# Kernel optimization log

Measured on AMD Instinct MI355X. Metric: run time of the kernel, lower is better.

Reference implementation:

```python
import jax, jax.numpy as jnp
import numpy as np

EPS = 1e-5

def layer_norm(x, gamma, beta):
    m = x.mean(axis=-1, keepdims=True)
    v = ((x - m) ** 2).mean(axis=-1, keepdims=True)  # correction=0
    return (x - m) / jnp.sqrt(v + EPS) * gamma + beta

def setup_inputs() -> dict:
    key = jax.random.key(0)
    B, T, E, H = 2, 2048, 1024, 16
    hd = E // H
    dff = 4 * E
    ks = jax.random.split(key, 10)
    s = 0.02
    return {
        "x": jax.random.normal(ks[0], (B, T, E), jnp.float32),
        "wq": jax.random.normal(ks[1], (H, E, hd), jnp.float32) * s,
        "wk": jax.random.normal(ks[2], (H, E, hd), jnp.float32) * s,
        "wv": jax.random.normal(ks[3], (H, E, hd), jnp.float32) * s,
        "w_proj": jax.random.normal(ks[4], (E, E), jnp.float32) * s,
        "b_proj": jnp.zeros((E,), jnp.float32),
        "gamma1": jnp.ones((E,), jnp.float32),
        "beta1": jnp.zeros((E,), jnp.float32),
        "gamma2": jnp.ones((E,), jnp.float32),
        "beta2": jnp.zeros((E,), jnp.float32),
        "w1": jax.random.normal(ks[5], (E, dff), jnp.float32) * s,
        "b1": jnp.zeros((dff,), jnp.float32),
        "w2": jax.random.normal(ks[6], (dff, E), jnp.float32) * s,
        "b2": jnp.zeros((E,), jnp.float32),
    }

def reference(x, wq, wk, wv, w_proj, b_proj, gamma1, beta1, gamma2, beta2, w1, b1, w2, b2):
    B, T, E = x.shape
    H, _, hd = wq.shape
    # pre-attention norm; NOTE: residual uses the normalized value (as in source)
    h = layer_norm(x, gamma1, beta1)
    # per-head projections, vectorized over heads: [B,H,T,hd]
    q = jnp.einsum('bte,hek->bhtk', h, wq)
    k = jnp.einsum('bte,hek->bhtk', h, wk)
    v = jnp.einsum('bte,hek->bhtk', h, wv)
    att = jnp.einsum('bhtk,bhsk->bhts', q, k) / jnp.sqrt(jnp.float32(hd))
    causal = jnp.tril(jnp.ones((T, T), bool))
    att = jnp.where(causal, att, -jnp.inf)
    p = jax.nn.softmax(att, axis=-1)  # dropout is identity in eval
    o = jnp.einsum('bhts,bhsk->bhtk', p, v)
    o = o.transpose(0, 2, 1, 3).reshape(B, T, E)  # concat heads
    attn_out = o @ w_proj + b_proj
    x2 = h + attn_out
    # pre-FFN norm; residual again uses normalized value
    h2 = layer_norm(x2, gamma2, beta2)
    ffn = jax.nn.relu(h2 @ w1 + b1) @ w2 + b2
    return h2 + ffn
```

## Files before the change

kernel.cpp:

```cpp
#include <hip/hip_runtime.h>
#include <stdint.h>

typedef unsigned short u16;
typedef __attribute__((ext_vector_type(8))) short short8;
typedef __attribute__((ext_vector_type(4))) short short4_t;
typedef __attribute__((ext_vector_type(4))) float f32x4;

__device__ __forceinline__ float b2f(u16 u){ union{unsigned i; float f;}v; v.i=((unsigned)u)<<16; return v.f; }
__device__ __forceinline__ u16 f2b(float f){ unsigned x=__float_as_uint(f); return (u16)((x + 0x7fffu + ((x>>16)&1u))>>16); }

#if __has_builtin(__builtin_amdgcn_exp2f)
#define EXP2F(x) __builtin_amdgcn_exp2f(x)
#else
#define EXP2F(x) exp2f(x)
#endif

#if __has_builtin(__builtin_amdgcn_mfma_f32_16x16x16_bf16)
#define MFMA16(a,b,c) __builtin_amdgcn_mfma_f32_16x16x16_bf16(a,b,c,0,0,0)
#elif __has_builtin(__builtin_amdgcn_mfma_f32_16x16x16bf16_1k)
#define MFMA16(a,b,c) __builtin_amdgcn_mfma_f32_16x16x16bf16_1k(a,b,c,0,0,0)
#else
static __device__ __forceinline__ f32x4 mfma16_asm(short4_t a, short4_t b, f32x4 c){
  __asm__("v_mfma_f32_16x16x16_bf16 %0, %1, %2, %3" : "=v"(c) : "v"(a), "v"(b), "0"(c));
  return c;
}
#define MFMA16(a,b,c) mfma16_asm(a,b,c)
#endif

__device__ __forceinline__ void async16(const void* g, void* l){
  __builtin_amdgcn_global_load_lds((const __attribute__((address_space(1))) void*)g,
                                   (__attribute__((address_space(3))) void*)l, 16, 0, 0);
}

__device__ __forceinline__ short4_t pack4(f32x4 s){
  unsigned u0 = (__float_as_uint(s[0]) + 0x8000u) >> 16;
  unsigned u1 = (__float_as_uint(s[1]) + 0x8000u) & 0xffff0000u;
  unsigned u2 = (__float_as_uint(s[2]) + 0x8000u) >> 16;
  unsigned u3 = (__float_as_uint(s[3]) + 0x8000u) & 0xffff0000u;
  union { unsigned v[2]; short4_t s4; } r;
  r.v[0] = u0 | u1; r.v[1] = u2 | u3;
  return r.s4;
}

template<int IN_F32>
__global__ __launch_bounds__(256) void ln_kernel(const void* __restrict__ xin,
    const float* __restrict__ g, const float* __restrict__ b, u16* __restrict__ y)
{
  const int E = 1024;
  int row = blockIdx.x, t = threadIdx.x;
  float f0,f1,f2,f3;
  if (IN_F32){
    const float* xr = (const float*)xin + (size_t)row*E;
    float4 xv = *(const float4*)(xr + t*4);
    f0=xv.x; f1=xv.y; f2=xv.z; f3=xv.w;
  } else {
    const u16* xr = (const u16*)xin + (size_t)row*E;
    ushort4 xv = *(const ushort4*)(xr + t*4);
    f0=b2f(xv.x); f1=b2f(xv.y); f2=b2f(xv.z); f3=b2f(xv.w);
  }
  float s1 = f0+f1+f2+f3;
  float s2 = f0*f0+f1*f1+f2*f2+f3*f3;
  #pragma unroll
  for (int off=32; off>=1; off>>=1){ s1 += __shfl_xor(s1,off); s2 += __shfl_xor(s2,off); }
  __shared__ float red[8];
  int w = t>>6;
  if ((t&63)==0){ red[w]=s1; red[4+w]=s2; }
  __syncthreads();
  float S1 = red[0]+red[1]+red[2]+red[3];
  float S2 = red[4]+red[5]+red[6]+red[7];
  float mean = S1*(1.0f/E);
  float var  = S2*(1.0f/E) - mean*mean;
  float inv  = rsqrtf(var + 1e-5f);
  float4 gv = *(const float4*)(g + t*4);
  float4 bv = *(const float4*)(b + t*4);
  ushort4 o;
  o.x = f2b((f0-mean)*inv*gv.x+bv.x);
  o.y = f2b((f1-mean)*inv*gv.y+bv.y);
  o.z = f2b((f2-mean)*inv*gv.z+bv.z);
  o.w = f2b((f3-mean)*inv*gv.w+bv.w);
  *(ushort4*)(y + (size_t)row*E + t*4) = o;
}

__global__ __launch_bounds__(256) void transpose_bt(const float* __restrict__ src, u16* __restrict__ dst,
                                                    int ld_src, int ld_dst)
{
  __shared__ u16 tile[64*66];
  int c0 = blockIdx.x*64, r0 = blockIdx.y*64;
  int t = threadIdx.x;
  #pragma unroll
  for (int i=0;i<16;++i){
    int lin = i*256 + t;
    int rr = lin>>6, cc = lin&63;
    tile[cc*66+rr] = f2b(src[(size_t)(r0+rr)*ld_src + c0+cc]);
  }
  __syncthreads();
  #pragma unroll
  for (int i=0;i<16;++i){
    int lin = i*256 + t;
    int cc = lin>>6, rr = lin&63;
    dst[(size_t)(c0+cc)*ld_dst + r0+rr] = tile[cc*66+rr];
  }
}

__global__ __launch_bounds__(256) void qkv_repack(const float* __restrict__ wq, const float* __restrict__ wk,
                                                  const float* __restrict__ wv, u16* __restrict__ dst)
{
  __shared__ u16 tile[64*66];
  int e0 = blockIdx.x*64;
  int sel = blockIdx.y>>4, h = blockIdx.y&15;
  const float* src = (sel==0?wq:(sel==1?wk:wv)) + (size_t)h*1024*64;
  int t = threadIdx.x;
  #pragma unroll
  for (int i=0;i<16;++i){
    int lin=i*256+t; int rr=lin>>6, cc=lin&63;
    tile[cc*66+rr] = f2b(src[(size_t)(e0+rr)*64 + cc]);
  }
  __syncthreads();
  #pragma unroll
  for (int i=0;i<16;++i){
    int lin=i*256+t; int cc=lin>>6, rr=lin&63;
    dst[(size_t)(sel*1024 + h*64 + cc)*1024 + e0+rr] = tile[cc*66+rr];
  }
}

__global__ __launch_bounds__(256) void vtrans(const u16* __restrict__ qkv, u16* __restrict__ VT)
{
  __shared__ u16 tile[64*66];
  int bh = blockIdx.y, bb = bh>>4, h = bh&15;
  int s0 = blockIdx.x*64;
  const u16* src = qkv + ((size_t)(bb*2048) + s0)*3072 + 2048 + h*64;
  int t = threadIdx.x;
  int sr = t>>3, c0 = (t&7)*8;
  #pragma unroll
  for (int half=0; half<2; ++half){
    const u16* p = src + (size_t)(sr+half*32)*3072 + c0;
    ushort4 v0 = *(const ushort4*)p;
    ushort4 v1 = *(const ushort4*)(p+4);
    uint* d = (uint*)(tile + (sr+half*32)*66 + c0);
    d[0] = (uint)v0.x | ((uint)v0.y<<16);
    d[1] = (uint)v0.z | ((uint)v0.w<<16);
    d[2] = (uint)v1.x | ((uint)v1.y<<16);
    d[3] = (uint)v1.z | ((uint)v1.w<<16);
  }
  __syncthreads();
  u16* out = VT + (size_t)bh*64*2048 + s0;
  int dw = t>>3, sc = (t&7)*8;
  #pragma unroll
  for (int half=0; half<2; ++half){
    int d = dw + half*32;
    short8 pk;
    #pragma unroll
    for (int j=0;j<8;++j) pk[j] = (short)tile[(sc+j)*66 + d];
    *(short8*)(out + (size_t)d*2048 + sc) = pk;
  }
}

__global__ __launch_bounds__(256, 4) void gemm64(const u16* __restrict__ A, const u16* __restrict__ Bt,
    u16* __restrict__ C, float* __restrict__ Cf, int M, int N, int K,
    const float* __restrict__ bias, const u16* __restrict__ residual, int do_relu, int gx)
{
  __shared__ __align__(16) u16 As[2][64*64];
  __shared__ __align__(16) u16 Bs[2][64*64];
  int t = threadIdx.x;
  int bid = blockIdx.y * gridDim.x + blockIdx.x;
  int xcd = bid & 7, slot = bid >> 3;
  int gy = 8 / gx;
  int rx = gridDim.x / gx, ry = gridDim.y / gy;
  int col_b = (xcd % gx) * rx + (slot % rx);
  int row_b = (xcd / gx) * ry + (slot / rx);
  int row0 = row_b*64, col0 = col_b*64;
  int l = t&63, w = t>>6;
  int lr = l&15, lq = l>>4;
  (void)M;

  f32x4 acc[4];
  #pragma unroll
  for (int j=0;j<4;++j) acc[j] = f32x4{0.f,0.f,0.f,0.f};

  const u16* gA = A  + (size_t)(row0 + (t>>3))*K + (((t&7)^((t>>3)&7))<<3);
  const u16* gB = Bt + (size_t)(col0 + (t>>3))*K + (((t&7)^((t>>3)&7))<<3);
  const size_t rnd = (size_t)32*K;
  int nk = K>>6;

  #pragma unroll
  for (int r=0;r<2;++r){
    async16(gA + r*rnd, As[0] + r*2048 + t*8);
    async16(gB + r*rnd, Bs[0] + r*2048 + t*8);
  }

  int sw8 = (lr&7);
  for (int kt=0; kt<nk; ++kt){
    int cur = kt&1;
    __syncthreads();
    if (kt+1 < nk){
      int ko = (kt+1)<<6;
      #pragma unroll
      for (int r=0;r<2;++r){
        async16(gA + r*rnd + ko, As[cur^1] + r*2048 + t*8);
        async16(gB + r*rnd + ko, Bs[cur^1] + r*2048 + t*8);
      }
    }
    const u16* as = As[cur];
    const u16* bs = Bs[cur];
    #pragma unroll
    for (int kk=0;kk<2;++kk){
      int so = (((kk*4+lq)^sw8))<<3;
      short8 a = *(const short8*)(as + (w*16+lr)*64 + so);
      short8 b[4];
      #pragma unroll
      for (int j=0;j<4;++j) b[j] = *(const short8*)(bs + (j*16+lr)*64 + so);
      #pragma unroll
      for (int j=0;j<4;++j)
        acc[j] = __builtin_amdgcn_mfma_f32_16x16x32_bf16(a, b[j], acc[j], 0,0,0);
    }
  }

  #pragma unroll
  for (int j=0;j<4;++j){
    int col = col0 + j*16 + lr;
    float bv = bias ? bias[col] : 0.0f;
    #pragma unroll
    for (int r=0;r<4;++r){
      int row = row0 + w*16 + lq*4 + r;
      float v = acc[j][r] + bv;
      if (do_relu) v = fmaxf(v, 0.0f);
      if (residual) v += b2f(residual[(size_t)row*N + col]);
      if (Cf) Cf[(size_t)row*N + col] = v;
      else    C [(size_t)row*N + col] = f2b(v);
    }
  }
}

__global__ __launch_bounds__(512,2) void gemm256(const u16* __restrict__ A, const u16* __restrict__ Bt,
    u16* __restrict__ C, float* __restrict__ Cf, int N, int K,
    const float* __restrict__ bias, const u16* __restrict__ residual, int do_relu, int gx)
{
  __shared__ __align__(16) u16 As[2][256*64];
  __shared__ __align__(16) u16 Bs[2][256*64];
  int t = threadIdx.x;
  int bid = blockIdx.y*gridDim.x + blockIdx.x;
  int xcd = bid & 7, slot = bid >> 3;
  int gy = 8/gx;
  int rx = gridDim.x/gx, ry = gridDim.y/gy;
  int col_b = (xcd%gx)*rx + slot%rx;
  int row_b = (xcd/gx)*ry + slot/rx;
  int row0 = row_b*256, col0 = col_b*256;
  int l = t&63, w = t>>6;
  int wr = w>>2, wc = w&3;
  int lr = l&15, lq = l>>4, sw = lr&7;

  f32x4 acc[8][4];
  #pragma unroll
  for (int m=0;m<8;++m)
    #pragma unroll
    for (int n=0;n<4;++n) acc[m][n] = f32x4{0.f,0.f,0.f,0.f};

  int i = t>>3, c8 = t&7;
  int swc = (c8 ^ (i&7))*8;
  const u16* aS[4]; const u16* bS[4];
  {
    int la[4] = { i, 128+i, 64+i, 192+i };
    #pragma unroll
    for (int s=0;s<4;++s){
      aS[s] = A + (size_t)(row0 + la[s])*K + swc;
      int p = s*64 + i;
      int lb = ((p>>5)&3)*64 + (p>>7)*32 + (p&31);
      bS[s] = Bt + (size_t)(col0 + lb)*K + swc;
    }
  }
  int nk = K>>6;

  u16* A0p = As[0]; u16* A1p = As[1];
  u16* B0p = Bs[0]; u16* B1p = Bs[1];

  short8 af[4][2], bP[2][2], bQ[2][2];

#define VM8  asm volatile("s_waitcnt vmcnt(8)" ::: "memory");
#define VM6  asm volatile("s_waitcnt vmcnt(6)" ::: "memory");
#define VM0  asm volatile("s_waitcnt vmcnt(0)" ::: "memory");
#define BAR  __builtin_amdgcn_s_barrier();

#define RD_A(BUF,qm) \
  _Pragma("unroll") \
  for (int mm=0;mm<4;++mm){ \
    _Pragma("unroll") \
    for (int kk=0;kk<2;++kk) \
      af[mm][kk] = *(const short8*)((const u16*)(BUF) + ((qm)*128 + wr*64 + mm*16 + lr)*64 + (((kk*4+lq)^sw)<<3)); \
  }
#define RD_B(DST,BUF,qn) \
  _Pragma("unroll") \
  for (int nn=0;nn<2;++nn){ \
    _Pragma("unroll") \
    for (int kk=0;kk<2;++kk) \
      DST[nn][kk] = *(const short8*)((const u16*)(BUF) + ((qn)*128 + wc*32 + nn*16 + lr)*64 + (((kk*4+lq)^sw)<<3)); \
  }
#define MMQ(qm,qn,BSS) \
  __builtin_amdgcn_s_setprio(1); \
  _Pragma("unroll") \
  for (int mm=0;mm<4;++mm){ \
    _Pragma("unroll") \
    for (int nn=0;nn<2;++nn){ \
      _Pragma("unroll") \
      for (int kk=0;kk<2;++kk) \
        acc[(qm)*4+mm][(qn)*2+nn] = __builtin_amdgcn_mfma_f32_16x16x32_bf16(af[mm][kk], BSS[nn][kk], acc[(qm)*4+mm][(qn)*2+nn], 0,0,0); \
    } \
  } \
  __builtin_amdgcn_s_setprio(0);

  async16(aS[0], A0p + 0*4096 + t*8);
  async16(aS[1], A0p + 1*4096 + t*8);
  async16(bS[0], B0p + 0*4096 + t*8);
  async16(bS[1], B0p + 1*4096 + t*8);
  async16(bS[2], B0p + 2*4096 + t*8);
  async16(bS[3], B0p + 3*4096 + t*8);
  async16(aS[2], A0p + 2*4096 + t*8);
  async16(aS[3], A0p + 3*4096 + t*8);
  async16(aS[0]+64, A1p + 0*4096 + t*8);
  async16(aS[1]+64, A1p + 1*4096 + t*8);
  async16(bS[0]+64, B1p + 0*4096 + t*8);
  async16(bS[1]+64, B1p + 1*4096 + t*8);
  async16(bS[2]+64, B1p + 2*4096 + t*8);
  async16(bS[3]+64, B1p + 3*4096 + t*8);
  VM8; BAR;
  RD_A(A0p, 0); RD_B(bP, B0p, 0);

  for (int kt=0; kt<nk-1; ++kt){
    int cur = kt&1;
    u16* Ac = As[cur]; u16* Bc = Bs[cur];
    u16* An = As[cur^1]; u16* Bn = Bs[cur^1];
    int ko1 = (kt+1)<<6;
    int kc2 = (kt+2 < nk) ? kt+2 : nk-1;
    int ko2 = kc2<<6;
    async16(aS[2]+ko1, An + 2*4096 + t*8);
    async16(aS[3]+ko1, An + 3*4096 + t*8);
    BAR;
    MMQ(0,0,bP);
    RD_B(bQ, Bc, 1);
    BAR;
    async16(bS[2]+ko2, Bc + 2*4096 + t*8);
    async16(bS[3]+ko2, Bc + 3*4096 + t*8);
    VM8; BAR;
    MMQ(0,1,bQ);
    RD_A(Ac, 1);
    BAR;
    async16(aS[0]+ko2, Ac + 0*4096 + t*8);
    async16(aS[1]+ko2, Ac + 1*4096 + t*8);
    BAR;
    MMQ(1,1,bQ);
    BAR;
    async16(bS[0]+ko2, Bc + 0*4096 + t*8);
    async16(bS[1]+ko2, Bc + 1*4096 + t*8);
    VM8; BAR;
    MMQ(1,0,bP);
    RD_A(An, 0); RD_B(bP, Bn, 0);
    BAR;
  }
  {
    int cur = (nk-1)&1;
    u16* Ac = As[cur]; u16* Bc = Bs[cur];
    BAR;
    MMQ(0,0,bP);
    RD_B(bQ, Bc, 1);
    BAR;
    VM6; BAR;
    MMQ(0,1,bQ);
    RD_A(Ac, 1);
    MMQ(1,1,bQ);
    MMQ(1,0,bP);
  }
  VM0;

#undef VM8
#undef VM6
#undef VM0
#undef BAR
#undef RD_A
#undef RD_B
#undef MMQ

  #pragma unroll
  for (int m=0;m<8;++m){
    #pragma unroll
    for (int n=0;n<4;++n){
      int col = col0 + wc*64 + n*16 + lr;
      float bv = bias ? bias[col] : 0.0f;
      #pragma unroll
      for (int r=0;r<4;++r){
        int row = row0 + wr*128 + m*16 + lq*4 + r;
        float v = acc[m][n][r] + bv;
        if (do_relu) v = fmaxf(v, 0.0f);
        if (residual) v += b2f(residual[(size_t)row*N + col]);
        if (Cf) Cf[(size_t)row*N + col] = v;
        else    C [(size_t)row*N + col] = f2b(v);
      }
    }
  }
}

__global__ __launch_bounds__(256,4) void attn_kernel(const u16* __restrict__ QKV,
    const u16* __restrict__ VT, u16* __restrict__ O)
{
  const int T=2048, LD=3072, E=1024;
  int bid = blockIdx.y * gridDim.x + blockIdx.x;
  int xcd = bid & 7, slot = bid >> 3;
  int idx = slot & 31, grp = slot >> 5;
  int qt = (grp & 1) ? idx : 31 - idx;
  int bh = xcd*4 + grp;
  int bb = bh>>4, h = bh&15;
  const u16* base = QKV + (size_t)bb*T*LD;
  const u16* Qp = base + h*64;
  const u16* Kp = base + 1024 + h*64;
  const u16* Vtp = VT + (size_t)bh*64*2048;
  int t = threadIdx.x, l = t&63, w = t>>6;
  int lr = l&15, lq = l>>4;

  __shared__ __align__(16) u16 Ks[2][64*64];
  __shared__ __align__(16) u16 Vs[2][64*64];

  const float QSC = 0.125f*1.44269504f;
  int q0 = qt*64 + w*16;
  short8 aq[2];
  #pragma unroll
  for (int kk=0;kk<2;++kk){
    short8 raw = *(const short8*)(Qp + (size_t)(q0+lr)*LD + kk*32 + lq*8);
    short8 sc;
    #pragma unroll
    for (int j=0;j<8;++j) sc[j] = (short)f2b(b2f((u16)raw[j])*QSC);
    aq[kk]=sc;
  }

  float mrun = -3e38f, lrun = 0.f;
  f32x4 Oacc[4];
  #pragma unroll
  for (int dt=0;dt<4;++dt) Oacc[dt] = f32x4{0.f,0.f,0.f,0.f};

  int kc = (l&7) ^ (l>>3);
  int ra = 8*w + (l>>3);

  async16(Kp  + (size_t)ra*LD        + kc*8, Ks[0] + t*8);
  async16(Kp  + (size_t)(ra+32)*LD   + kc*8, Ks[0] + 2048 + t*8);
  async16(Vtp + (size_t)ra*2048      + kc*8, Vs[0] + t*8);
  async16(Vtp + (size_t)(ra+32)*2048 + kc*8, Vs[0] + 2048 + t*8);

  for (int it=0; it<=qt; ++it){
    int s0 = it*64, cur = it&1;
    __syncthreads();
    if (it < qt){
      int sn = s0+64;
      u16* kd = Ks[cur^1]; u16* vd = Vs[cur^1];
      async16(Kp  + (size_t)(sn+ra)*LD        + kc*8, kd + t*8);
      async16(Kp  + (size_t)(sn+ra+32)*LD     + kc*8, kd + 2048 + t*8);
      async16(Vtp + (size_t)ra*2048      + sn + kc*8, vd + t*8);
      async16(Vtp + (size_t)(ra+32)*2048 + sn + kc*8, vd + 2048 + t*8);
    }
    const u16* ks = Ks[cur];
    const u16* vs = Vs[cur];

    f32x4 S[4];
    #pragma unroll
    for (int st=0; st<4; ++st){
      short8 kf0 = *(const short8*)(ks + (st*16+lr)*64 + ((lq  )^(lr&7))*8);
      short8 kf1 = *(const short8*)(ks + (st*16+lr)*64 + ((4+lq)^(lr&7))*8);
      f32x4 z = f32x4{0.f,0.f,0.f,0.f};
      z = __builtin_amdgcn_mfma_f32_16x16x32_bf16(kf0, aq[0], z, 0,0,0);
      z = __builtin_amdgcn_mfma_f32_16x16x32_bf16(kf1, aq[1], z, 0,0,0);
      S[st] = z;
    }
    if (it == qt){
      int qg = q0 + lr;
      #pragma unroll
      for (int st=0;st<4;++st)
        #pragma unroll
        for (int r=0;r<4;++r){
          int sg = s0 + st*16 + lq*4 + r;
          if (sg > qg) S[st][r] = -3e38f;
        }
    }
    float m = S[0][0];
    #pragma unroll
    for (int st=0;st<4;++st)
      #pragma unroll
      for (int r=0;r<4;++r) m = fmaxf(m, S[st][r]);
    m = fmaxf(m, __shfl_xor(m,16));
    m = fmaxf(m, __shfl_xor(m,32));
    float mnew = fmaxf(mrun, m);
    float alpha = EXP2F(mrun - mnew);
    mrun = mnew;
    float ssum = 0.f;
    #pragma unroll
    for (int st=0;st<4;++st)
      #pragma unroll
      for (int r=0;r<4;++r){ float p = EXP2F(S[st][r]-mnew); S[st][r]=p; ssum+=p; }
    ssum += __shfl_xor(ssum,16);
    ssum += __shfl_xor(ssum,32);
    lrun = lrun*alpha + ssum;
    short4_t pk[4];
    #pragma unroll
    for (int st=0;st<4;++st) pk[st] = pack4(S[st]);
    float af[4];
    #pragma unroll
    for (int r=0;r<4;++r) af[r] = __shfl(alpha, lq*4+r);
    #pragma unroll
    for (int dt=0;dt<4;++dt)
      #pragma unroll
      for (int r=0;r<4;++r) Oacc[dt][r] *= af[r];
    #pragma unroll
    for (int st=0;st<4;++st){
      #pragma unroll
      for (int dt=0;dt<4;++dt){
        short4_t vf = *(const short4_t*)(vs + (dt*16+lr)*64 + ((2*st+(lq>>1))^(lr&7))*8 + (lq&1)*4);
        Oacc[dt] = MFMA16(pk[st], vf, Oacc[dt]);
      }
    }
  }
  float linv[4];
  #pragma unroll
  for (int r=0;r<4;++r) linv[r] = 1.0f/__shfl(lrun, lq*4+r);
  #pragma unroll
  for (int dt=0;dt<4;++dt)
    #pragma unroll
    for (int r=0;r<4;++r){
      int qg = q0 + lq*4 + r;
      O[(size_t)(bb*T+qg)*E + h*64 + dt*16 + lr] = f2b(Oacc[dt][r]*linv[r]);
    }
}

extern "C" void kernel_launch(void* const* d_in, const int* in_sizes, int n_in,
                              void* d_out, int out_size, void* d_ws, size_t ws_size,
                              hipStream_t stream)
{
  (void)in_sizes; (void)n_in; (void)out_size; (void)ws_size;
  const float* x     = (const float*)d_in[0];
  const float* wq    = (const float*)d_in[1];
  const float* wk    = (const float*)d_in[2];
  const float* wv    = (const float*)d_in[3];
  const float* wproj = (const float*)d_in[4];
  const float* bproj = (const float*)d_in[5];
  const float* g1    = (const float*)d_in[6];
  const float* be1   = (const float*)d_in[7];
  const float* g2    = (const float*)d_in[8];
  const float* be2   = (const float*)d_in[9];
  const float* w1    = (const float*)d_in[10];
  const float* b1    = (const float*)d_in[11];
  const float* w2    = (const float*)d_in[12];
  const float* b2    = (const float*)d_in[13];
  float* out = (float*)d_out;

  char* ws = (char*)d_ws;
  size_t off = 0;
  auto alloc = [&](size_t bytes)->void*{ void* p = ws + off; off += (bytes + 255) & ~(size_t)255; return p; };
  u16* hnorm  = (u16*)alloc((size_t)4096*1024*2);
  u16* qkv    = (u16*)alloc((size_t)4096*3072*2);
  u16* VT     = (u16*)alloc((size_t)32*64*2048*2);
  u16* attnO  = (u16*)alloc((size_t)4096*1024*2);
  u16* x2     = (u16*)alloc((size_t)4096*1024*2);
  u16* h2     = (u16*)alloc((size_t)4096*1024*2);
  u16* ffn1   = (u16*)alloc((size_t)4096*4096*2);
  u16* wqkvT  = (u16*)alloc((size_t)3072*1024*2);
  u16* wprojT = (u16*)alloc((size_t)1024*1024*2);
  u16* w1T    = (u16*)alloc((size_t)4096*1024*2);
  u16* w2T    = (u16*)alloc((size_t)1024*4096*2);

  qkv_repack  <<<dim3(16,48),256,0,stream>>>(wq,wk,wv,wqkvT);
  transpose_bt<<<dim3(16,16),256,0,stream>>>(wproj, wprojT, 1024, 1024);
  transpose_bt<<<dim3(64,16),256,0,stream>>>(w1,    w1T,    4096, 1024);
  transpose_bt<<<dim3(16,64),256,0,stream>>>(w2,    w2T,    1024, 4096);

  ln_kernel<1><<<4096,256,0,stream>>>(x, g1, be1, hnorm);
  gemm256<<<dim3(12,16),512,0,stream>>>(hnorm, wqkvT, qkv, nullptr, 3072, 1024, nullptr, nullptr, 0, 4);
  vtrans<<<dim3(32,32),256,0,stream>>>(qkv, VT);
  attn_kernel<<<dim3(32,32),256,0,stream>>>(qkv, VT, attnO);
  gemm64<<<dim3(16,64),256,0,stream>>>(attnO, wprojT, x2, nullptr, 4096,1024,1024, bproj, hnorm, 0, 4);
  ln_kernel<0><<<4096,256,0,stream>>>(x2, g2, be2, h2);
  gemm256<<<dim3(16,16),512,0,stream>>>(h2, w1T, ffn1, nullptr, 4096, 1024, b1, nullptr, 1, 4);
  gemm64<<<dim3(16,64),256,0,stream>>>(ffn1, w2T, nullptr, out, 4096,1024,4096, b2, h2, 0, 4);
}
```

Baseline: 348.2 us.

## Process two query subtiles per attention block to reuse K/V tiles

```diff
diff --git a/kernel.cpp b/kernel.cpp
--- a/kernel.cpp
+++ b/kernel.cpp
@@ -397,14 +397,14 @@
   }
 }
 
-__global__ __launch_bounds__(256,4) void attn_kernel(const u16* __restrict__ QKV,
+__global__ __launch_bounds__(256,2) void attn_kernel(const u16* __restrict__ QKV,
     const u16* __restrict__ VT, u16* __restrict__ O)
 {
   const int T=2048, LD=3072, E=1024;
   int bid = blockIdx.y * gridDim.x + blockIdx.x;
   int xcd = bid & 7, slot = bid >> 3;
-  int idx = slot & 31, grp = slot >> 5;
-  int qt = (grp & 1) ? idx : 31 - idx;
+  int idx = slot & 15, grp = slot >> 4;
+  int qt = ((grp>>1)&1) ? idx : 15 - idx;
   int bh = xcd*4 + grp;
   int bb = bh>>4, h = bh&15;
   const u16* base = QKV + (size_t)bb*T*LD;
@@ -418,21 +418,26 @@
   __shared__ __align__(16) u16 Vs[2][64*64];
 
   const float QSC = 0.125f*1.44269504f;
-  int q0 = qt*64 + w*16;
-  short8 aq[2];
+  int q0 = qt*128 + w*16;
+  short8 aq0[2], aq1[2];
   #pragma unroll
   for (int kk=0;kk<2;++kk){
-    short8 raw = *(const short8*)(Qp + (size_t)(q0+lr)*LD + kk*32 + lq*8);
-    short8 sc;
-    #pragma unroll
-    for (int j=0;j<8;++j) sc[j] = (short)f2b(b2f((u16)raw[j])*QSC);
-    aq[kk]=sc;
-  }
-
-  float mrun = -3e38f, lrun = 0.f;
-  f32x4 Oacc[4];
-  #pragma unroll
-  for (int dt=0;dt<4;++dt) Oacc[dt] = f32x4{0.f,0.f,0.f,0.f};
+    short8 r0 = *(const short8*)(Qp + (size_t)(q0+lr)*LD    + kk*32 + lq*8);
+    short8 r1 = *(const short8*)(Qp + (size_t)(q0+64+lr)*LD + kk*32 + lq*8);
+    short8 s0v, s1v;
+    #pragma unroll
+    for (int j=0;j<8;++j){
+      s0v[j] = (short)f2b(b2f((u16)r0[j])*QSC);
+      s1v[j] = (short)f2b(b2f((u16)r1[j])*QSC);
+    }
+    aq0[kk]=s0v; aq1[kk]=s1v;
+  }
+
+  float mrun0 = -3e38f, lrun0 = 0.f;
+  float mrun1 = -3e38f, lrun1 = 0.f;
+  f32x4 O0[4], O1[4];
+  #pragma unroll
+  for (int dt=0;dt<4;++dt){ O0[dt] = f32x4{0.f,0.f,0.f,0.f}; O1[dt] = f32x4{0.f,0.f,0.f,0.f}; }
 
   int kc = (l&7) ^ (l>>3);
   int ra = 8*w + (l>>3);
@@ -442,10 +447,11 @@
   async16(Vtp + (size_t)ra*2048      + kc*8, Vs[0] + t*8);
   async16(Vtp + (size_t)(ra+32)*2048 + kc*8, Vs[0] + 2048 + t*8);
 
-  for (int it=0; it<=qt; ++it){
+  int itmax = 2*qt + 1;
+  for (int it=0; it<=itmax; ++it){
     int s0 = it*64, cur = it&1;
     __syncthreads();
-    if (it < qt){
+    if (it < itmax){
       int sn = s0+64;
       u16* kd = Ks[cur^1]; u16* vd = Vs[cur^1];
       async16(Kp  + (size_t)(sn+ra)*LD        + kc*8, kd + t*8);
@@ -456,72 +462,122 @@
     const u16* ks = Ks[cur];
     const u16* vs = Vs[cur];
 
-    f32x4 S[4];
+    f32x4 S0[4], S1[4];
     #pragma unroll
     for (int st=0; st<4; ++st){
       short8 kf0 = *(const short8*)(ks + (st*16+lr)*64 + ((lq  )^(lr&7))*8);
       short8 kf1 = *(const short8*)(ks + (st*16+lr)*64 + ((4+lq)^(lr&7))*8);
-      f32x4 z = f32x4{0.f,0.f,0.f,0.f};
-      z = __builtin_amdgcn_mfma_f32_16x16x32_bf16(kf0, aq[0], z, 0,0,0);
-      z = __builtin_amdgcn_mfma_f32_16x16x32_bf16(kf1, aq[1], z, 0,0,0);
-      S[st] = z;
-    }
-    if (it == qt){
+      f32x4 z0 = f32x4{0.f,0.f,0.f,0.f};
+      f32x4 z1 = f32x4{0.f,0.f,0.f,0.f};
+      z0 = __builtin_amdgcn_mfma_f32_16x16x32_bf16(kf0, aq0[0], z0, 0,0,0);
+      z0 = __builtin_amdgcn_mfma_f32_16x16x32_bf16(kf1, aq0[1], z0, 0,0,0);
+      z1 = __builtin_amdgcn_mfma_f32_16x16x32_bf16(kf0, aq1[0], z1, 0,0,0);
+      z1 = __builtin_amdgcn_mfma_f32_16x16x32_bf16(kf1, aq1[1], z1, 0,0,0);
+      S0[st] = z0; S1[st] = z1;
+    }
+    if (it >= 2*qt){
       int qg = q0 + lr;
       #pragma unroll
       for (int st=0;st<4;++st)
         #pragma unroll
         for (int r=0;r<4;++r){
           int sg = s0 + st*16 + lq*4 + r;
-          if (sg > qg) S[st][r] = -3e38f;
+          if (sg > qg) S0[st][r] = -3e38f;
         }
     }
-    float m = S[0][0];
-    #pragma unroll
-    for (int st=0;st<4;++st)
-      #pragma unroll
-      for (int r=0;r<4;++r) m = fmaxf(m, S[st][r]);
-    m = fmaxf(m, __shfl_xor(m,16));
-    m = fmaxf(m, __shfl_xor(m,32));
-    float mnew = fmaxf(mrun, m);
-    float alpha = EXP2F(mrun - mnew);
-    mrun = mnew;
-    float ssum = 0.f;
-    #pragma unroll
-    for (int st=0;st<4;++st)
-      #pragma unroll
-      for (int r=0;r<4;++r){ float p = EXP2F(S[st][r]-mnew); S[st][r]=p; ssum+=p; }
-    ssum += __shfl_xor(ssum,16);
-    ssum += __shfl_xor(ssum,32);
-    lrun = lrun*alpha + ssum;
-    short4_t pk[4];
-    #pragma unroll
-    for (int st=0;st<4;++st) pk[st] = pack4(S[st]);
-    float af[4];
-    #pragma unroll
-    for (int r=0;r<4;++r) af[r] = __shfl(alpha, lq*4+r);
-    #pragma unroll
-    for (int dt=0;dt<4;++dt)
-      #pragma unroll
-      for (int r=0;r<4;++r) Oacc[dt][r] *= af[r];
+    if (it == itmax){
+      int qg = q0 + 64 + lr;
+      #pragma unroll
+      for (int st=0;st<4;++st)
+        #pragma unroll
+        for (int r=0;r<4;++r){
+          int sg = s0 + st*16 + lq*4 + r;
+          if (sg > qg) S1[st][r] = -3e38f;
+        }
+    }
+    short4_t pk0[4], pk1[4];
+    {
+      float m = S0[0][0];
+      #pragma unroll
+      for (int st=0;st<4;++st)
+        #pragma unroll
+        for (int r=0;r<4;++r) m = fmaxf(m, S0[st][r]);
+      m = fmaxf(m, __shfl_xor(m,16));
+      m = fmaxf(m, __shfl_xor(m,32));
+      float mnew = fmaxf(mrun0, m);
+      float alpha = EXP2F(mrun0 - mnew);
+      mrun0 = mnew;
+      float ssum = 0.f;
+      #pragma unroll
+      for (int st=0;st<4;++st)
+        #pragma unroll
+        for (int r=0;r<4;++r){ float p = EXP2F(S0[st][r]-mnew); S0[st][r]=p; ssum+=p; }
+      ssum += __shfl_xor(ssum,16);
+      ssum += __shfl_xor(ssum,32);
+      lrun0 = lrun0*alpha + ssum;
+      #pragma unroll
+      for (int st=0;st<4;++st) pk0[st] = pack4(S0[st]);
+      float af[4];
+      #pragma unroll
+      for (int r=0;r<4;++r) af[r] = __shfl(alpha, lq*4+r);
+      #pragma unroll
+      for (int dt=0;dt<4;++dt)
+        #pragma unroll
+        for (int r=0;r<4;++r) O0[dt][r] *= af[r];
+    }
+    {
+      float m = S1[0][0];
+      #pragma unroll
+      for (int st=0;st<4;++st)
+        #pragma unroll
+        for (int r=0;r<4;++r) m = fmaxf(m, S1[st][r]);
+      m = fmaxf(m, __shfl_xor(m,16));
+      m = fmaxf(m, __shfl_xor(m,32));
+      float mnew = fmaxf(mrun1, m);
+      float alpha = EXP2F(mrun1 - mnew);
+      mrun1 = mnew;
+      float ssum = 0.f;
+      #pragma unroll
+      for (int st=0;st<4;++st)
+        #pragma unroll
+        for (int r=0;r<4;++r){ float p = EXP2F(S1[st][r]-mnew); S1[st][r]=p; ssum+=p; }
+      ssum += __shfl_xor(ssum,16);
+      ssum += __shfl_xor(ssum,32);
+      lrun1 = lrun1*alpha + ssum;
+      #pragma unroll
+      for (int st=0;st<4;++st) pk1[st] = pack4(S1[st]);
+      float af[4];
+      #pragma unroll
+      for (int r=0;r<4;++r) af[r] = __shfl(alpha, lq*4+r);
+      #pragma unroll
+      for (int dt=0;dt<4;++dt)
+        #pragma unroll
+        for (int r=0;r<4;++r) O1[dt][r] *= af[r];
+    }
     #pragma unroll
     for (int st=0;st<4;++st){
       #pragma unroll
       for (int dt=0;dt<4;++dt){
         short4_t vf = *(const short4_t*)(vs + (dt*16+lr)*64 + ((2*st+(lq>>1))^(lr&7))*8 + (lq&1)*4);
-        Oacc[dt] = MFMA16(pk[st], vf, Oacc[dt]);
+        O0[dt] = MFMA16(pk0[st], vf, O0[dt]);
+        O1[dt] = MFMA16(pk1[st], vf, O1[dt]);
       }
     }
   }
-  float linv[4];
-  #pragma unroll
-  for (int r=0;r<4;++r) linv[r] = 1.0f/__shfl(lrun, lq*4+r);
+  float linv0[4], linv1[4];
+  #pragma unroll
+  for (int r=0;r<4;++r){
+    linv0[r] = 1.0f/__shfl(lrun0, lq*4+r);
+    linv1[r] = 1.0f/__shfl(lrun1, lq*4+r);
+  }
   #pragma unroll
   for (int dt=0;dt<4;++dt)
     #pragma unroll
     for (int r=0;r<4;++r){
-      int qg = q0 + lq*4 + r;
-      O[(size_t)(bb*T+qg)*E + h*64 + dt*16 + lr] = f2b(Oacc[dt][r]*linv[r]);
+      int qa = q0 + lq*4 + r;
+      int qb = q0 + 64 + lq*4 + r;
+      O[(size_t)(bb*T+qa)*E + h*64 + dt*16 + lr] = f2b(O0[dt][r]*linv0[r]);
+      O[(size_t)(bb*T+qb)*E + h*64 + dt*16 + lr] = f2b(O1[dt][r]*linv1[r]);
     }
 }
 
@@ -569,7 +625,7 @@
   ln_kernel<1><<<4096,256,0,stream>>>(x, g1, be1, hnorm);
   gemm256<<<dim3(12,16),512,0,stream>>>(hnorm, wqkvT, qkv, nullptr, 3072, 1024, nullptr, nullptr, 0, 4);
   vtrans<<<dim3(32,32),256,0,stream>>>(qkv, VT);
-  attn_kernel<<<dim3(32,32),256,0,stream>>>(qkv, VT, attnO);
+  attn_kernel<<<dim3(16,32),256,0,stream>>>(qkv, VT, attnO);
   gemm64<<<dim3(16,64),256,0,stream>>>(attnO, wprojT, x2, nullptr, 4096,1024,1024, bproj, hnorm, 0, 4);
   ln_kernel<0><<<4096,256,0,stream>>>(x2, g2, be2, h2);
   gemm256<<<dim3(16,16),512,0,stream>>>(h2, w1T, ffn1, nullptr, 4096, 1024, b1, nullptr, 1, 4);
```

New measurement: 357.8 us. 2.8% more time.
